# Performance work log

Hardware: AMD Instinct MI355X
Metric: run time of the kernel (lower is better)

Reference implementation:

```python
import jax, jax.numpy as jnp
import numpy as np

EPS = 1e-5


def _selective_scan(u, delta, A, Bm, Cm, D, delta_bias):
    # u, delta: (B, KD, L); A: (KD, N); Bm, Cm: (B, K, N, L); D, delta_bias: (KD,)
    Bb, KD, L = u.shape
    K = Bm.shape[1]
    Din = KD // K
    N = A.shape[1]
    delta = jax.nn.softplus(delta + delta_bias[None, :, None])            # (B,KD,L)
    dA = jnp.exp(delta[..., None] * A[None, :, None, :])                  # (B,KD,L,N)
    Bl = jnp.broadcast_to(Bm[:, :, None], (Bb, K, Din, N, L)).reshape(Bb, KD, N, L)
    Bl = jnp.moveaxis(Bl, -1, 2)                                          # (B,KD,L,N)
    dBu = (delta * u)[..., None] * Bl                                     # (B,KD,L,N)

    def comb(c1, c2):
        a1, b1 = c1
        a2, b2 = c2
        return a2 * a1, a2 * b1 + b2

    _, h = jax.lax.associative_scan(comb, (dA, dBu), axis=2)              # h: (B,KD,L,N)
    Cl = jnp.broadcast_to(Cm[:, :, None], (Bb, K, Din, N, L)).reshape(Bb, KD, N, L)
    Cl = jnp.moveaxis(Cl, -1, 2)
    y = jnp.sum(h * Cl, axis=-1) + D[None, :, None] * u                   # (B,KD,L)
    return y


def setup_inputs() -> dict:
    key = jax.random.key(0)
    ks = jax.random.split(key, 12)
    B, H, W, Dd = 1, 16, 16, 16
    C = 48            # d_model
    Din = 48          # d_inner (expand=1)
    N = 16            # d_state
    R = 3             # dt_rank = ceil(48/16)
    K = 8             # scan directions
    x = jax.random.normal(ks[0], (B, H, W, Dd, C), jnp.float32)
    in_proj_w = jax.random.normal(ks[1], (2 * Din, C), jnp.float32) * (C ** -0.5)
    conv_w = jax.random.normal(ks[2], (Din, 1, 3, 3, 3), jnp.float32) * 0.1
    conv_b = jax.random.normal(ks[3], (Din,), jnp.float32) * 0.01
    x_proj_weight = jax.random.normal(ks[4], (K, R + 2 * N, Din), jnp.float32) * (Din ** -0.5)
    dt_projs_weight = jax.random.uniform(ks[5], (K, Din, R), jnp.float32, -(R ** -0.5), R ** -0.5)
    # faithful dt bias init: inverse softplus of dt ~ logU(1e-3, 1e-1)
    u = jax.random.uniform(ks[6], (K, Din), jnp.float32)
    dt = jnp.exp(u * (np.log(0.1) - np.log(0.001)) + np.log(0.001))
    dt = jnp.clip(dt, 1e-4, None)
    dt_projs_bias = dt + jnp.log(-jnp.expm1(-dt))
    A_logs = jnp.log(jnp.broadcast_to(jnp.arange(1, N + 1, dtype=jnp.float32), (K * Din, N))).copy()
    Ds = jnp.ones((K * Din,), jnp.float32)
    norm_w = jnp.ones((Din,), jnp.float32)
    norm_b = jnp.zeros((Din,), jnp.float32)
    out_proj_w = jax.random.normal(ks[7], (C, Din), jnp.float32) * (Din ** -0.5)
    return {"x": x, "in_proj_w": in_proj_w, "conv_w": conv_w, "conv_b": conv_b,
            "x_proj_weight": x_proj_weight, "dt_projs_weight": dt_projs_weight,
            "dt_projs_bias": dt_projs_bias, "A_logs": A_logs, "Ds": Ds,
            "norm_w": norm_w, "norm_b": norm_b, "out_proj_w": out_proj_w}


def reference(x, in_proj_w, conv_w, conv_b, x_proj_weight, dt_projs_weight,
              dt_projs_bias, A_logs, Ds, norm_w, norm_b, out_proj_w):
    Bb, H, W, Dd, C = x.shape
    Din = in_proj_w.shape[0] // 2
    K = x_proj_weight.shape[0]
    R = dt_projs_weight.shape[2]
    N = A_logs.shape[1]
    L = H * W * Dd
    # in_proj and gate split
    xz = jnp.einsum('bhwdc,ec->bhwde', x, in_proj_w)
    xm, z = jnp.split(xz, 2, axis=-1)
    # depthwise 3D conv + SiLU (channels-first)
    xc = jnp.transpose(xm, (0, 4, 1, 2, 3))                               # (B,Din,H,W,D)
    xc = jax.lax.conv_general_dilated(xc, conv_w, (1, 1, 1), 'SAME',
                                      dimension_numbers=('NCDHW', 'OIDHW', 'NCDHW'),
                                      feature_group_count=Din)
    xc = jax.nn.silu(xc + conv_b[None, :, None, None, None])
    # 8 scan orderings: 4 axis permutations + their reversals
    x0 = xc.reshape(Bb, Din, L)
    x1 = jnp.transpose(xc, (0, 1, 3, 2, 4)).reshape(Bb, Din, L)
    x2 = jnp.transpose(xc, (0, 1, 4, 3, 2)).reshape(Bb, Din, L)
    x3 = jnp.transpose(xc, (0, 1, 2, 4, 3)).reshape(Bb, Din, L)
    x4s = jnp.stack([x0, x1, x2, x3], axis=1)                             # (B,4,Din,L)
    xs = jnp.concatenate([x4s, jnp.flip(x4s, axis=-1)], axis=1)           # (B,8,Din,L)
    # per-direction projections
    x_dbl = jnp.einsum('bkdl,kcd->bkcl', xs, x_proj_weight)
    dts, Bs, Cs = jnp.split(x_dbl, [R, R + N], axis=2)                    # (B,K,R,L),(B,K,N,L),(B,K,N,L)
    dts = jnp.einsum('bkrl,kdr->bkdl', dts, dt_projs_weight)              # (B,K,Din,L)
    u = xs.reshape(Bb, K * Din, L)
    delta = dts.reshape(Bb, K * Din, L)
    A = -jnp.exp(A_logs)                                                  # (K*Din, N)
    y = _selective_scan(u, delta, A, Bs, Cs, Ds, dt_projs_bias.reshape(-1))
    y = y.reshape(Bb, K, Din, L)
    # undo reversals and permutations, sum all directions
    yk = y[:, :4] + jnp.flip(y[:, 4:], axis=-1)                           # (B,4,Din,L)
    y0 = yk[:, 0].reshape(Bb, Din, H, W, Dd)
    y1 = jnp.transpose(yk[:, 1].reshape(Bb, Din, W, H, Dd), (0, 1, 3, 2, 4))
    y2 = jnp.transpose(yk[:, 2].reshape(Bb, Din, Dd, W, H), (0, 1, 4, 3, 2))
    y3 = jnp.transpose(yk[:, 3].reshape(Bb, Din, H, Dd, W), (0, 1, 2, 4, 3))
    ysum = y0 + y1 + y2 + y3                                              # (B,Din,H,W,D)
    # LayerNorm over channels, gate, out_proj
    yl = jnp.transpose(ysum, (0, 2, 3, 4, 1))                             # (B,H,W,D,Din)
    mu = jnp.mean(yl, axis=-1, keepdims=True)
    var = jnp.mean((yl - mu) ** 2, axis=-1, keepdims=True)
    yn = (yl - mu) * jax.lax.rsqrt(var + EPS) * norm_w + norm_b
    out = yn * jax.nn.silu(z)
    return jnp.einsum('bhwde,ce->bhwdc', out, out_proj_w)
```

## Files before the change

### kernel.cpp

```cpp
#include <hip/hip_runtime.h>
#include <hip/hip_bf16.h>
#include <math.h>

#define HH 16
#define WW 16
#define DD 16
#define LL 4096
#define CC 48
#define DIN 48
#define NN 16
#define RR 3
#define KK 8
#define KD 384
#define NCH 64
#define CHL 64

__global__ __launch_bounds__(256) void k_inproj(const float* __restrict__ x,
                                                const float* __restrict__ W,
                                                float* __restrict__ xm,
                                                float* __restrict__ z) {
    int tid = blockIdx.x * 256 + threadIdx.x;
    if (tid >= LL * 96) return;
    int e = tid % 96, l = tid / 96;
    const float4* xr = (const float4*)(x + l * CC);
    const float4* wr = (const float4*)(W + e * CC);
    float acc = 0.f;
#pragma unroll
    for (int c4 = 0; c4 < CC / 4; ++c4) {
        float4 a = xr[c4], b = wr[c4];
        acc += a.x * b.x + a.y * b.y + a.z * b.z + a.w * b.w;
    }
    if (e < DIN) xm[e * LL + l] = acc;
    else         z[l * DIN + (e - DIN)] = acc;
}

__global__ __launch_bounds__(256) void k_convscat(const float* __restrict__ xm,
                                                  const float* __restrict__ cw,
                                                  const float* __restrict__ cb,
                                                  float* __restrict__ xs) {
    int tid = blockIdx.x * 256 + threadIdx.x;
    if (tid >= DIN * LL) return;
    int s = tid & (LL - 1), d = tid >> 12;
    int dd = s & 15, w = (s >> 4) & 15, h = s >> 8;
    const float* wp = cw + d * 27;
    const float* xp = xm + d * LL;
    float acc = 0.f;
#pragma unroll
    for (int i = -1; i <= 1; ++i) {
        int hh = h + i; if (hh < 0 || hh > 15) continue;
#pragma unroll
        for (int j = -1; j <= 1; ++j) {
            int ww2 = w + j; if (ww2 < 0 || ww2 > 15) continue;
#pragma unroll
            for (int q = -1; q <= 1; ++q) {
                int dd2 = dd + q; if (dd2 < 0 || dd2 > 15) continue;
                acc += wp[(i + 1) * 9 + (j + 1) * 3 + (q + 1)]
                     * xp[hh * 256 + ww2 * 16 + dd2];
            }
        }
    }
    acc += cb[d];
    float v = acc / (1.f + __expf(-acc));
    int p0 = s;
    int p1 = w * 256 + h * 16 + dd;
    int p2 = dd * 256 + w * 16 + h;
    int p3 = h * 256 + dd * 16 + w;
    xs[(size_t)(0 * DIN + d) * LL + p0] = v;
    xs[(size_t)(1 * DIN + d) * LL + p1] = v;
    xs[(size_t)(2 * DIN + d) * LL + p2] = v;
    xs[(size_t)(3 * DIN + d) * LL + p3] = v;
    xs[(size_t)(4 * DIN + d) * LL + (LL - 1 - p0)] = v;
    xs[(size_t)(5 * DIN + d) * LL + (LL - 1 - p1)] = v;
    xs[(size_t)(6 * DIN + d) * LL + (LL - 1 - p2)] = v;
    xs[(size_t)(7 * DIN + d) * LL + (LL - 1 - p3)] = v;
}

__global__ __launch_bounds__(768) void k_xscan1(const float* __restrict__ xs,
                                                const float* __restrict__ xpw,
                                                const float* __restrict__ dtw,
                                                const float* __restrict__ dtb,
                                                const float* __restrict__ A_logs,
                                                float* __restrict__ BC,
                                                float* __restrict__ dsp,
                                                float* __restrict__ pa_g,
                                                float* __restrict__ hf_g) {
    int k = blockIdx.x >> 6;
    int c = blockIdx.x & (NCH - 1);
    int l0 = c * CHL;
    int tid = threadIdx.x;
    __shared__ float xt[48 * 68];
    __shared__ float xd[35 * 65];
    __shared__ float wl[35 * 49];
    __shared__ float dt[48 * 68];
    for (int i = tid; i < 35 * 48; i += 768)
        wl[(i / 48) * 49 + (i % 48)] = xpw[k * 35 * 48 + i];
    {
        int d = tid >> 4, w = tid & 15;
        float4 v = ((const float4*)(xs + (size_t)(k * DIN + d) * LL + l0))[w];
        ((float4*)(xt + d * 68))[w] = v;
    }
    __syncthreads();
    if (tid < 560) {
        int cc = tid % 35, l4 = tid / 35;
        const float* wr = wl + cc * 49;
        float4 acc = {0.f, 0.f, 0.f, 0.f};
#pragma unroll
        for (int d2 = 0; d2 < 48; ++d2) {
            float4 v = ((const float4*)(xt + d2 * 68))[l4];
            float w = wr[d2];
            acc.x += v.x * w; acc.y += v.y * w; acc.z += v.z * w; acc.w += v.w * w;
        }
        float* o = xd + cc * 65 + l4 * 4;
        o[0] = acc.x; o[1] = acc.y; o[2] = acc.z; o[3] = acc.w;
    }
    __syncthreads();
    if (tid < 512) {
        int l = tid >> 3, q = tid & 7;
        float4 v;
#pragma unroll
        for (int j = 0; j < 4; ++j) (&v.x)[j] = xd[(3 + q * 4 + j) * 65 + l];
        ((float4*)(BC + ((size_t)(k * LL + l0 + l)) * 32))[q] = v;
    }
#pragma unroll
    for (int r = 0; r < 4; ++r) {
        int idx = r * 768 + tid;
        int d2 = idx >> 6, l = idx & 63;
        int gd = k * DIN + d2;
        float v = xd[l] * dtw[gd * 3] + xd[65 + l] * dtw[gd * 3 + 1]
                + xd[130 + l] * dtw[gd * 3 + 2] + dtb[gd];
        float sp = (v > 20.f) ? v : log1pf(__expf(v));
        dt[d2 * 68 + l] = sp;
        dsp[(size_t)gd * LL + l0 + l] = sp;
    }
    __syncthreads();
    int d = tid >> 4, n = tid & 15;
    int gid = k * DIN + d;
    float A = -__expf(A_logs[gid * NN + n]);
    float h = 0.f, pa = 1.f;
#pragma unroll 4
    for (int i = 0; i < CHL; ++i) {
        float delta = dt[d * 68 + i];
        float u = xt[d * 68 + i];
        float Bv = xd[(3 + n) * 65 + i];
        float dA = __expf(delta * A);
        h = h * dA + delta * u * Bv;
        pa *= dA;
    }
    size_t si = (size_t)gid * (NCH * 16) + c * 16 + n;
    pa_g[si] = pa;
    hf_g[si] = h;
}

__global__ __launch_bounds__(256) void k_scan2(const float* __restrict__ pa_g,
                                               const float* __restrict__ hf_g,
                                               float* __restrict__ h0_g) {
    int t = blockIdx.x * 256 + threadIdx.x;
    if (t >= KD * NN) return;
    int n = t & 15;
    int gid = t >> 4;
    size_t base = (size_t)gid * (NCH * 16) + n;
    float h = 0.f;
#pragma unroll 4
    for (int c = 0; c < NCH; ++c) {
        size_t idx = base + (size_t)c * 16;
        h0_g[idx] = h;
        h = h * pa_g[idx] + hf_g[idx];
    }
}

__global__ __launch_bounds__(768) void k_scan3(const float* __restrict__ xs,
                                               const float* __restrict__ dsp,
                                               const float* __restrict__ BC,
                                               const float* __restrict__ A_logs,
                                               const float* __restrict__ Ds,
                                               const float* __restrict__ h0_g,
                                               float* __restrict__ y2) {
    int k = blockIdx.x >> 6;
    int c = blockIdx.x & (NCH - 1);
    int l0 = c * CHL;
    int tid = threadIdx.x;
    int d = tid >> 4, n = tid & 15;
    int gid = k * DIN + d;
    __shared__ float y_t[48 * 68];
    float A = -__expf(A_logs[gid * NN + n]);
    float Dv = Ds[gid];
    float h = h0_g[(size_t)gid * (NCH * 16) + c * 16 + n];
    const float* up = xs + (size_t)gid * LL + l0;
    const float* dp = dsp + (size_t)gid * LL + l0;
    const float* bp = BC + ((size_t)(k * LL + l0)) * 32 + n;
    const float* cp = bp + 16;
#pragma unroll 4
    for (int i = 0; i < CHL; ++i) {
        float delta = dp[i];
        float u = up[i];
        float Bv = bp[(size_t)i * 32];
        float Cv = cp[(size_t)i * 32];
        float dA = __expf(delta * A);
        h = h * dA + delta * u * Bv;
        float p = h * Cv;
        p += __shfl_xor(p, 1, 64);
        p += __shfl_xor(p, 2, 64);
        p += __shfl_xor(p, 4, 64);
        p += __shfl_xor(p, 8, 64);
        if (n == 0) y_t[d * 68 + i] = p + Dv * u;
    }
    __syncthreads();
    {
        int g = tid >> 6, l = tid & 63;
        int lg = l0 + l;
        int ll = (k & 4) ? (LL - 1 - lg) : lg;
        int a = ll >> 8, b2 = (ll >> 4) & 15, c2 = ll & 15;
        int s;
        switch (k & 3) {
            case 0: s = ll;                        break;
            case 1: s = b2 * 256 + a * 16 + c2;    break;
            case 2: s = c2 * 256 + b2 * 16 + a;    break;
            default: s = a * 256 + c2 * 16 + b2;   break;
        }
        float4 v;
#pragma unroll
        for (int j = 0; j < 4; ++j) (&v.x)[j] = y_t[(g * 4 + j) * 68 + l];
        ((float4*)(y2 + (size_t)s * KD + k * DIN))[g] = v;
    }
}

__global__ __launch_bounds__(256) void k_final2(const float* __restrict__ y2,
                                                const float* __restrict__ z,
                                                const float* __restrict__ nw,
                                                const float* __restrict__ nb,
                                                const float* __restrict__ opw,
                                                float* __restrict__ out) {
    int wv = threadIdx.x >> 6, lane = threadIdx.x & 63;
    int s = blockIdx.x * 4 + wv;
    __shared__ float g[4][DIN];
    float val = 0.f;
    if (lane < DIN) {
        const float* yp = y2 + (size_t)s * KD + lane;
#pragma unroll
        for (int k = 0; k < KK; ++k) val += yp[k * DIN];
    }
    float m = val;
#pragma unroll
    for (int o = 32; o >= 1; o >>= 1) m += __shfl_xor(m, o, 64);
    m *= (1.f / 48.f);
    float dv = (lane < DIN) ? (val - m) : 0.f;
    float v2 = dv * dv;
#pragma unroll
    for (int o = 32; o >= 1; o >>= 1) v2 += __shfl_xor(v2, o, 64);
    v2 *= (1.f / 48.f);
    float inv = rsqrtf(v2 + 1e-5f);
    if (lane < DIN) {
        float yn = dv * inv * nw[lane] + nb[lane];
        float zz = z[s * DIN + lane];
        g[wv][lane] = yn * (zz / (1.f + __expf(-zz)));
    }
    __syncthreads();
    if (lane < DIN) {
        const float* wr = opw + lane * DIN;
        float acc = 0.f;
#pragma unroll
        for (int e = 0; e < DIN; ++e) acc += g[wv][e] * wr[e];
        out[s * CC + lane] = acc;
    }
}

extern "C" void kernel_launch(void* const* d_in, const int* in_sizes, int n_in,
                              void* d_out, int out_size, void* d_ws, size_t ws_size,
                              hipStream_t stream) {
    const float* x      = (const float*)d_in[0];
    const float* ipw    = (const float*)d_in[1];
    const float* cw     = (const float*)d_in[2];
    const float* cb     = (const float*)d_in[3];
    const float* xpw    = (const float*)d_in[4];
    const float* dtw    = (const float*)d_in[5];
    const float* dtb    = (const float*)d_in[6];
    const float* A_logs = (const float*)d_in[7];
    const float* Ds     = (const float*)d_in[8];
    const float* nw     = (const float*)d_in[9];
    const float* nb     = (const float*)d_in[10];
    const float* opw    = (const float*)d_in[11];
    float* out = (float*)d_out;

    float* ws   = (float*)d_ws;
    float* xm   = ws;
    float* z    = xm + DIN * LL;
    float* xs   = z + LL * DIN;
    float* BC   = xs + (size_t)KD * LL;
    float* dsp  = BC + (size_t)KK * LL * 32;
    float* y2   = dsp + (size_t)KD * LL;
    float* pa_g = y2 + (size_t)LL * KD;
    float* hf_g = pa_g + (size_t)KD * NCH * 16;
    float* h0_g = hf_g + (size_t)KD * NCH * 16;

    k_inproj<<<(LL * 96 + 255) / 256, 256, 0, stream>>>(x, ipw, xm, z);
    k_convscat<<<(DIN * LL + 255) / 256, 256, 0, stream>>>(xm, cw, cb, xs);
    k_xscan1<<<KK * NCH, 768, 0, stream>>>(xs, xpw, dtw, dtb, A_logs,
                                           BC, dsp, pa_g, hf_g);
    k_scan2<<<(KD * NN + 255) / 256, 256, 0, stream>>>(pa_g, hf_g, h0_g);
    k_scan3<<<KK * NCH, 768, 0, stream>>>(xs, dsp, BC, A_logs, Ds, h0_g, y2);
    k_final2<<<LL / 4, 256, 0, stream>>>(y2, z, nw, nb, opw, out);
}
```

Measured before the change: 167.9 us.

## Gather scan inputs in xscan1, interleave u/delta, use DPP row reductions

The conv kernel now writes a single channel-major activation buffer, and xscan1 gathers each direction's permuted or reversed sequence directly from it instead of reading an 8-way scattered copy. u and softplus(delta) are stored interleaved as float2 so the scan kernels do one load per step. The 16-lane reduction in scan3 uses DPP row operations instead of shuffles, the scan loops are unrolled further, and the x_proj weights are read from global memory rather than staged in LDS. The gathered reads in xscan1 are strided and uncoalesced, which may offset the bytes saved by dropping the scatter.

```diff
diff --git a/kernel.cpp b/kernel.cpp
--- a/kernel.cpp
+++ b/kernel.cpp
@@ -15,6 +15,25 @@
 #define NCH 64
 #define CHL 64
 
+__device__ __forceinline__ float dpp_add(float x, const int ctrl_tag) {
+    int xi = __float_as_int(x);
+    int yi;
+    switch (ctrl_tag) {
+        case 0: yi = __builtin_amdgcn_update_dpp(0, xi, 0xB1, 0xF, 0xF, true); break;
+        case 1: yi = __builtin_amdgcn_update_dpp(0, xi, 0x4E, 0xF, 0xF, true); break;
+        case 2: yi = __builtin_amdgcn_update_dpp(0, xi, 0x124, 0xF, 0xF, true); break;
+        default: yi = __builtin_amdgcn_update_dpp(0, xi, 0x128, 0xF, 0xF, true); break;
+    }
+    return x + __int_as_float(yi);
+}
+__device__ __forceinline__ float row16_sum(float p) {
+    p = dpp_add(p, 0);
+    p = dpp_add(p, 1);
+    p = dpp_add(p, 2);
+    p = dpp_add(p, 3);
+    return p;
+}
+
 __global__ __launch_bounds__(256) void k_inproj(const float* __restrict__ x,
                                                 const float* __restrict__ W,
                                                 float* __restrict__ xm,
@@ -34,10 +53,10 @@
     else         z[l * DIN + (e - DIN)] = acc;
 }
 
-__global__ __launch_bounds__(256) void k_convscat(const float* __restrict__ xm,
-                                                  const float* __restrict__ cw,
-                                                  const float* __restrict__ cb,
-                                                  float* __restrict__ xs) {
+__global__ __launch_bounds__(256) void k_conv(const float* __restrict__ xm,
+                                              const float* __restrict__ cw,
+                                              const float* __restrict__ cb,
+                                              float* __restrict__ xc) {
     int tid = blockIdx.x * 256 + threadIdx.x;
     if (tid >= DIN * LL) return;
     int s = tid & (LL - 1), d = tid >> 12;
@@ -60,28 +79,16 @@
         }
     }
     acc += cb[d];
-    float v = acc / (1.f + __expf(-acc));
-    int p0 = s;
-    int p1 = w * 256 + h * 16 + dd;
-    int p2 = dd * 256 + w * 16 + h;
-    int p3 = h * 256 + dd * 16 + w;
-    xs[(size_t)(0 * DIN + d) * LL + p0] = v;
-    xs[(size_t)(1 * DIN + d) * LL + p1] = v;
-    xs[(size_t)(2 * DIN + d) * LL + p2] = v;
-    xs[(size_t)(3 * DIN + d) * LL + p3] = v;
-    xs[(size_t)(4 * DIN + d) * LL + (LL - 1 - p0)] = v;
-    xs[(size_t)(5 * DIN + d) * LL + (LL - 1 - p1)] = v;
-    xs[(size_t)(6 * DIN + d) * LL + (LL - 1 - p2)] = v;
-    xs[(size_t)(7 * DIN + d) * LL + (LL - 1 - p3)] = v;
-}
-
-__global__ __launch_bounds__(768) void k_xscan1(const float* __restrict__ xs,
+    xc[tid] = acc / (1.f + __expf(-acc));
+}
+
+__global__ __launch_bounds__(768) void k_xscan1(const float* __restrict__ xc,
                                                 const float* __restrict__ xpw,
                                                 const float* __restrict__ dtw,
                                                 const float* __restrict__ dtb,
                                                 const float* __restrict__ A_logs,
                                                 float* __restrict__ BC,
-                                                float* __restrict__ dsp,
+                                                float* __restrict__ ud_g,
                                                 float* __restrict__ pa_g,
                                                 float* __restrict__ hf_g) {
     int k = blockIdx.x >> 6;
@@ -90,19 +97,28 @@
     int tid = threadIdx.x;
     __shared__ float xt[48 * 68];
     __shared__ float xd[35 * 65];
-    __shared__ float wl[35 * 49];
-    __shared__ float dt[48 * 68];
-    for (int i = tid; i < 35 * 48; i += 768)
-        wl[(i / 48) * 49 + (i % 48)] = xpw[k * 35 * 48 + i];
-    {
-        int d = tid >> 4, w = tid & 15;
-        float4 v = ((const float4*)(xs + (size_t)(k * DIN + d) * LL + l0))[w];
-        ((float4*)(xt + d * 68))[w] = v;
+    __shared__ float2 ud[48 * 68];
+    int kperm = k & 3, krev = k & 4;
+#pragma unroll
+    for (int r = 0; r < 4; ++r) {
+        int item = r * 768 + tid;
+        int d = item >> 6, i = item & 63;
+        int lg = l0 + i;
+        int ll = krev ? (LL - 1 - lg) : lg;
+        int a = ll >> 8, b2 = (ll >> 4) & 15, c2 = ll & 15;
+        int src;
+        switch (kperm) {
+            case 0: src = ll;                       break;
+            case 1: src = b2 * 256 + a * 16 + c2;   break;
+            case 2: src = c2 * 256 + b2 * 16 + a;   break;
+            default: src = a * 256 + c2 * 16 + b2;  break;
+        }
+        xt[d * 68 + i] = xc[d * LL + src];
     }
     __syncthreads();
     if (tid < 560) {
         int cc = tid % 35, l4 = tid / 35;
-        const float* wr = wl + cc * 49;
+        const float* wr = xpw + (k * 35 + cc) * DIN;
         float4 acc = {0.f, 0.f, 0.f, 0.f};
 #pragma unroll
         for (int d2 = 0; d2 < 48; ++d2) {
@@ -123,27 +139,28 @@
     }
 #pragma unroll
     for (int r = 0; r < 4; ++r) {
-        int idx = r * 768 + tid;
-        int d2 = idx >> 6, l = idx & 63;
+        int item = r * 768 + tid;
+        int d2 = item >> 6, l = item & 63;
         int gd = k * DIN + d2;
         float v = xd[l] * dtw[gd * 3] + xd[65 + l] * dtw[gd * 3 + 1]
                 + xd[130 + l] * dtw[gd * 3 + 2] + dtb[gd];
         float sp = (v > 20.f) ? v : log1pf(__expf(v));
-        dt[d2 * 68 + l] = sp;
-        dsp[(size_t)gd * LL + l0 + l] = sp;
+        float u = xt[d2 * 68 + l];
+        float2 p = make_float2(u, sp);
+        ud[d2 * 68 + l] = p;
+        ((float2*)ud_g)[(size_t)gd * LL + l0 + l] = p;
     }
     __syncthreads();
     int d = tid >> 4, n = tid & 15;
     int gid = k * DIN + d;
     float A = -__expf(A_logs[gid * NN + n]);
     float h = 0.f, pa = 1.f;
-#pragma unroll 4
+#pragma unroll 8
     for (int i = 0; i < CHL; ++i) {
-        float delta = dt[d * 68 + i];
-        float u = xt[d * 68 + i];
+        float2 uv = ud[d * 68 + i];
         float Bv = xd[(3 + n) * 65 + i];
-        float dA = __expf(delta * A);
-        h = h * dA + delta * u * Bv;
+        float dA = __expf(uv.y * A);
+        h = h * dA + uv.y * uv.x * Bv;
         pa *= dA;
     }
     size_t si = (size_t)gid * (NCH * 16) + c * 16 + n;
@@ -168,8 +185,7 @@
     }
 }
 
-__global__ __launch_bounds__(768) void k_scan3(const float* __restrict__ xs,
-                                               const float* __restrict__ dsp,
+__global__ __launch_bounds__(768) void k_scan3(const float* __restrict__ ud_g,
                                                const float* __restrict__ BC,
                                                const float* __restrict__ A_logs,
                                                const float* __restrict__ Ds,
@@ -185,24 +201,18 @@
     float A = -__expf(A_logs[gid * NN + n]);
     float Dv = Ds[gid];
     float h = h0_g[(size_t)gid * (NCH * 16) + c * 16 + n];
-    const float* up = xs + (size_t)gid * LL + l0;
-    const float* dp = dsp + (size_t)gid * LL + l0;
+    const float2* up = ((const float2*)ud_g) + (size_t)gid * LL + l0;
     const float* bp = BC + ((size_t)(k * LL + l0)) * 32 + n;
     const float* cp = bp + 16;
-#pragma unroll 4
+#pragma unroll 8
     for (int i = 0; i < CHL; ++i) {
-        float delta = dp[i];
-        float u = up[i];
+        float2 uv = up[i];
         float Bv = bp[(size_t)i * 32];
         float Cv = cp[(size_t)i * 32];
-        float dA = __expf(delta * A);
-        h = h * dA + delta * u * Bv;
-        float p = h * Cv;
-        p += __shfl_xor(p, 1, 64);
-        p += __shfl_xor(p, 2, 64);
-        p += __shfl_xor(p, 4, 64);
-        p += __shfl_xor(p, 8, 64);
-        if (n == 0) y_t[d * 68 + i] = p + Dv * u;
+        float dA = __expf(uv.y * A);
+        h = h * dA + uv.y * uv.x * Bv;
+        float p = row16_sum(h * Cv);
+        if (n == 0) y_t[d * 68 + i] = p + Dv * uv.x;
     }
     __syncthreads();
     {
@@ -284,19 +294,19 @@
     float* ws   = (float*)d_ws;
     float* xm   = ws;
     float* z    = xm + DIN * LL;
-    float* xs   = z + LL * DIN;
-    float* BC   = xs + (size_t)KD * LL;
-    float* dsp  = BC + (size_t)KK * LL * 32;
-    float* y2   = dsp + (size_t)KD * LL;
+    float* xc   = z + LL * DIN;
+    float* ud_g = xc + DIN * LL;
+    float* BC   = ud_g + (size_t)2 * KD * LL;
+    float* y2   = BC + (size_t)KK * LL * 32;
     float* pa_g = y2 + (size_t)LL * KD;
     float* hf_g = pa_g + (size_t)KD * NCH * 16;
     float* h0_g = hf_g + (size_t)KD * NCH * 16;
 
     k_inproj<<<(LL * 96 + 255) / 256, 256, 0, stream>>>(x, ipw, xm, z);
-    k_convscat<<<(DIN * LL + 255) / 256, 256, 0, stream>>>(xm, cw, cb, xs);
-    k_xscan1<<<KK * NCH, 768, 0, stream>>>(xs, xpw, dtw, dtb, A_logs,
-                                           BC, dsp, pa_g, hf_g);
+    k_conv<<<(DIN * LL + 255) / 256, 256, 0, stream>>>(xm, cw, cb, xc);
+    k_xscan1<<<KK * NCH, 768, 0, stream>>>(xc, xpw, dtw, dtb, A_logs,
+                                           BC, ud_g, pa_g, hf_g);
     k_scan2<<<(KD * NN + 255) / 256, 256, 0, stream>>>(pa_g, hf_g, h0_g);
-    k_scan3<<<KK * NCH, 768, 0, stream>>>(xs, dsp, BC, A_logs, Ds, h0_g, y2);
+    k_scan3<<<KK * NCH, 768, 0, stream>>>(ud_g, BC, A_logs, Ds, h0_g, y2);
     k_final2<<<LL / 4, 256, 0, stream>>>(y2, z, nw, nb, opw, out);
 }
```

Result: faster. 155.0 us (-7.7%).
